# Kernel tuning notes

Hardware: AMD Instinct MI355X
Metric: run time of the kernel (lower is better)

Reference implementation:

```python
import jax, jax.numpy as jnp
import numpy as np

B, N, D, A = 256, 32, 128, 16
DOA, E, FD, H, O = 144, 128, 128, 256, 1  # obs_act_in, obs_out/embed, final_in, hidden, final_out


def setup_inputs() -> dict:
    key = jax.random.key(0)
    ks = jax.random.split(key, 12)
    p = lambda k, shape: jax.random.normal(k, shape, jnp.float32) * 0.05
    return {
        "states": jax.random.normal(ks[0], (B, N, D), jnp.float32),
        "policies": jax.random.uniform(ks[1], (B, N, A), dtype=jnp.float32),
        "actions": jax.random.uniform(ks[2], (B, N, A), dtype=jnp.float32),
        "Wk_proc": p(ks[3], (D, E)),
        "Wq_proc": p(ks[4], (D, E)),
        "Wv_proc": p(ks[5], (D, E)),
        "Wk": p(ks[6], (E, FD)),
        "Wq": p(ks[7], (E, FD)),
        "We": p(ks[8], (DOA, E)),
        "Wav": p(ks[9], (E, FD)),
        "W1": p(ks[10], (FD, H)),
        "W2": p(ks[11], (H, O)),
    }


def reference(states, policies, actions, Wk_proc, Wq_proc, Wv_proc, Wk, Wq, We, Wav, W1, W2):
    n = states.shape[1]
    # NOTE: original code divides BOTH attention stages by sqrt(self.d_k_obs) = final_input_dim
    scale = 1.0 / jnp.sqrt(jnp.asarray(Wk.shape[1], states.dtype))

    # stage-1 attention over agents [B,N,N]
    k1 = states @ Wk_proc
    q1 = states @ Wq_proc
    v1 = states @ Wv_proc
    w1 = jax.nn.softmax(jnp.einsum('bie,bje->bij', q1, k1) * scale, axis=-1)
    wav1 = jnp.einsum('bij,bje->bie', w1, v1)  # [B,N,E]

    # stage-2 attention weights
    k2 = wav1 @ Wk
    q2 = wav1 @ Wq
    w2 = jax.nn.softmax(jnp.einsum('bif,bjf->bij', q2, k2) * scale, axis=-1)

    # build obs-action/policy tensor: entry [b,i,j] uses policy of agent j when i==j else action of j
    oa = jnp.concatenate([states, actions], axis=-1)   # [B,N,DOA]
    op = jnp.concatenate([states, policies], axis=-1)  # [B,N,DOA]
    eye = jnp.eye(n, dtype=states.dtype)[:, :, None]   # [N,N,1]
    oap = eye * op[:, None, :, :] + (1.0 - eye) * oa[:, None, :, :]  # [B,N,N,DOA]

    av = (oap @ We) @ Wav  # [B,N,N,FD]

    # node_features[b,i,j,f] = sum_k w2[b,i,k] * av[b,j,k,f]  (avoids the 5D repeat)
    node = jnp.einsum('bik,bjkf->bijf', w2, av)

    h = node @ W1
    h = jnp.where(h > 0, h, 0.01 * h)  # leaky_relu, default slope
    value = h @ W2  # [B,N,N,O]
    return value, w1, w2
```

## Files before the change

### kernel.cpp

```cpp
#include <hip/hip_runtime.h>
#include <math.h>

#define NB 256
#define NN 32
#define DD 128
#define NA 16
#define HH 256

using f32x4v  = __attribute__((ext_vector_type(4))) float;
using bf16x8  = __attribute__((ext_vector_type(8))) short;

static __device__ __forceinline__ float4 ld4(const float* p){ return *reinterpret_cast<const float4*>(p); }
static __device__ __forceinline__ void st4f(float* p, float4 v){ *reinterpret_cast<float4*>(p) = v; }
static __device__ __forceinline__ float elem(float4 v, int kk){
    return (kk==0)?v.x:(kk==1)?v.y:(kk==2)?v.z:v.w;
}

static __device__ __forceinline__ unsigned f2bf(float x){
    unsigned u = __float_as_uint(x);
    u += 0x7fffu + ((u >> 16) & 1u);
    return u >> 16;
}
static __device__ __forceinline__ unsigned pack2(float a, float b){
    return f2bf(a) | (f2bf(b) << 16);
}

static __device__ __forceinline__ f32x4v mfma16(bf16x8 a, bf16x8 b, f32x4v c){
    return __builtin_amdgcn_mfma_f32_16x16x32_bf16(a, b, c, 0, 0, 0);
}

static __device__ __forceinline__ bf16x8 to_bf8(const float v[8]){
    union { bf16x8 v8; unsigned u[4]; } r;
    #pragma unroll
    for (int j = 0; j < 4; j++) r.u[j] = pack2(v[2*j], v[2*j+1]);
    return r.v8;
}

static __device__ __forceinline__ void store_frag(unsigned short* __restrict__ dst,
                                                  int frag, int l, const float v[8]){
    uint4 p;
    p.x = pack2(v[0], v[1]); p.y = pack2(v[2], v[3]);
    p.z = pack2(v[4], v[5]); p.w = pack2(v[6], v[7]);
    *reinterpret_cast<uint4*>(dst + (size_t)(frag*64 + l)*8) = p;
}

__global__ __launch_bounds__(512)
void k_pre(const float* __restrict__ We, const float* __restrict__ Wav,
           const float* __restrict__ W1,
           const float* __restrict__ Wqp, const float* __restrict__ Wkp,
           const float* __restrict__ Wvp, const float* __restrict__ Wq,
           const float* __restrict__ Wk,
           float* __restrict__ WABf, unsigned short* __restrict__ WABs,
           unsigned short* __restrict__ Wqps, unsigned short* __restrict__ Wkps,
           unsigned short* __restrict__ Wvqs, unsigned short* __restrict__ Wvks)
{
    __shared__ float SH[5120];
    const int t = threadIdx.x;
    const int bid = blockIdx.x;
    const int l   = t & 63;
    const int wvv = t >> 6;
    const int lg  = l >> 4;
    const int lc  = l & 15;

    if (bid < 16) {
        float* T2f  = SH;
        float* WABt = SH + 2560;
        const int ct = bid;
        {
            const int arow = wvv*16 + lc;
            f32x4v acc = {0.f,0.f,0.f,0.f};
            #pragma unroll
            for (int kt = 0; kt < 4; kt++) {
                const float* ap = Wav + (size_t)arow*128 + kt*32 + lg*8;
                float4 a0 = ld4(ap), a1 = ld4(ap + 4);
                float av8[8] = {a0.x,a0.y,a0.z,a0.w,a1.x,a1.y,a1.z,a1.w};
                const float* bp = W1 + (size_t)(kt*32 + lg*8)*256 + ct*16 + lc;
                float bv8[8];
                #pragma unroll
                for (int i = 0; i < 8; i++) bv8[i] = bp[(size_t)i*256];
                acc = mfma16(to_bf8(av8), to_bf8(bv8), acc);
            }
            const int dr = wvv*16 + lg*4;
            #pragma unroll
            for (int r = 0; r < 4; r++) T2f[(dr+r)*20 + lc] = acc[r];
        }
        __syncthreads();
        #pragma unroll
        for (int pass = 0; pass < 2; pass++) {
            const int mt9 = (pass == 0) ? wvv : 8 + wvv;
            if (pass == 1 && wvv >= 2) continue;
            const int arow = mt9*16 + lc;
            f32x4v acc = {0.f,0.f,0.f,0.f};
            #pragma unroll
            for (int kt = 0; kt < 4; kt++) {
                float av8[8];
                if (arow < 144) {
                    const float* ap = We + (size_t)arow*128 + kt*32 + lg*8;
                    float4 a0 = ld4(ap), a1 = ld4(ap + 4);
                    av8[0]=a0.x; av8[1]=a0.y; av8[2]=a0.z; av8[3]=a0.w;
                    av8[4]=a1.x; av8[5]=a1.y; av8[6]=a1.z; av8[7]=a1.w;
                } else {
                    #pragma unroll
                    for (int i = 0; i < 8; i++) av8[i] = 0.f;
                }
                float bv8[8];
                #pragma unroll
                for (int i = 0; i < 8; i++) bv8[i] = T2f[(kt*32 + lg*8 + i)*20 + lc];
                acc = mfma16(to_bf8(av8), to_bf8(bv8), acc);
            }
            const int dr = mt9*16 + lg*4;
            #pragma unroll
            for (int r = 0; r < 4; r++) WABt[(dr+r)*16 + lc] = acc[r];
            if (mt9 == 8) {
                #pragma unroll
                for (int r = 0; r < 4; r++)
                    WABf[(size_t)(dr+r)*256 + ct*16 + lc] = acc[r];
            }
        }
        __syncthreads();
        if (t < 320) {
            int kt = t >> 6, ll = t & 63;
            float v[8];
            #pragma unroll
            for (int i = 0; i < 8; i++)
                v[i] = WABt[(kt*32 + (ll>>4)*8 + i)*16 + (ll&15)];
            store_frag(WABs, kt*16 + ct, ll, v);
        }
    } else if (bid < 24) {
        const int bb = bid - 16;
        const int fg = bb*8 + (t >> 6);
        const int sel = fg >> 5, frag = fg & 31;
        const int kt = frag >> 3, nt = frag & 7;
        const float* W = (sel==0) ? Wqp : Wkp;
        unsigned short* dst = (sel==0) ? Wqps : Wkps;
        float v[8];
        #pragma unroll
        for (int i = 0; i < 8; i++)
            v[i] = W[(kt*32 + (l>>4)*8 + i)*128 + nt*16 + (l&15)];
        store_frag(dst, frag, l, v);
    } else {
        float* T2f = SH;
        const int ct = (bid - 24) & 7;
        const float* Bsrc = (bid < 32) ? Wq : Wk;
        unsigned short* dst = (bid < 32) ? Wvqs : Wvks;
        {
            const int arow = wvv*16 + lc;
            f32x4v acc = {0.f,0.f,0.f,0.f};
            #pragma unroll
            for (int kt = 0; kt < 4; kt++) {
                const float* ap = Wvp + (size_t)arow*128 + kt*32 + lg*8;
                float4 a0 = ld4(ap), a1 = ld4(ap + 4);
                float av8[8] = {a0.x,a0.y,a0.z,a0.w,a1.x,a1.y,a1.z,a1.w};
                const float* bp = Bsrc + (size_t)(kt*32 + lg*8)*128 + ct*16 + lc;
                float bv8[8];
                #pragma unroll
                for (int i = 0; i < 8; i++) bv8[i] = bp[(size_t)i*128];
                acc = mfma16(to_bf8(av8), to_bf8(bv8), acc);
            }
            const int dr = wvv*16 + lg*4;
            #pragma unroll
            for (int r = 0; r < 4; r++) T2f[(dr+r)*20 + lc] = acc[r];
        }
        __syncthreads();
        if (t < 256) {
            int kt = t >> 6, ll = t & 63;
            float v[8];
            #pragma unroll
            for (int i = 0; i < 8; i++)
                v[i] = T2f[(kt*32 + (ll>>4)*8 + i)*20 + (ll&15)];
            store_frag(dst, kt*8 + ct, ll, v);
        }
    }
}

static __device__ __forceinline__ void scores_softmax512(const float* __restrict__ Qm,
                                                         const float* __restrict__ Km,
                                                         float scale,
                                                         float* __restrict__ w_lds,
                                                         float* __restrict__ w_out,
                                                         int i, int j)
{
    float s0 = 0.f, s1 = 0.f;
    #pragma unroll 4
    for (int k=0;k<128;k+=4){
        float4 qv = ld4(Qm + i*132 + k);
        float4 k0 = ld4(Km + j*132 + k);
        float4 k1 = ld4(Km + (j+16)*132 + k);
        s0 += qv.x*k0.x + qv.y*k0.y + qv.z*k0.z + qv.w*k0.w;
        s1 += qv.x*k1.x + qv.y*k1.y + qv.z*k1.z + qv.w*k1.w;
    }
    s0 *= scale; s1 *= scale;
    float m = fmaxf(s0, s1);
    #pragma unroll
    for (int d=1; d<16; d<<=1) m = fmaxf(m, __shfl_xor(m, d));
    float e0 = expf(s0 - m), e1 = expf(s1 - m);
    float sum = e0 + e1;
    #pragma unroll
    for (int d=1; d<16; d<<=1) sum += __shfl_xor(sum, d);
    float inv = 1.f / sum;
    e0 *= inv; e1 *= inv;
    w_lds[i*36 + j]      = e0;
    w_lds[i*36 + j + 16] = e1;
    w_out[i*32 + j]      = e0;
    w_out[i*32 + j + 16] = e1;
}

__global__ __launch_bounds__(512)
void k_main(const float* __restrict__ states, const float* __restrict__ pol,
            const float* __restrict__ act,
            const unsigned short* __restrict__ Wqps, const unsigned short* __restrict__ Wkps,
            const unsigned short* __restrict__ Wvqs, const unsigned short* __restrict__ Wvks,
            const unsigned short* __restrict__ WABs, const float* __restrict__ WABf,
            const float* __restrict__ W2,
            float* __restrict__ out_v, float* __restrict__ out_w1,
            float* __restrict__ out_w2)
{
    const int b = blockIdx.x;
    const int t = threadIdx.x;
    const float scale = 0.08838834764831845f;

    __shared__ float SH[15360];
    float* B1   = SH;
    float* B2   = SH + 4224;
    float* Wb1f = SH + 8448;
    float* Wb2f = SH + 9600;
    float* APd  = SH + 10752;
    unsigned short* Xoa = (unsigned short*)(SH + 11264);
    float*    A1 = SH;
    unsigned* P2 = (unsigned*)(SH + 11264);
    unsigned* Q2 = (unsigned*)SH;
    float* SPQ = Wb1f;

    const float* stg  = states + (size_t)b*(NN*DD);
    const float* actg = act + (size_t)b*(NN*NA);
    const float* polg = pol + (size_t)b*(NN*NA);

    const int l   = t & 63;
    const int wvv = t >> 6;
    const int lg  = l >> 4;
    const int lc  = l & 15;

    {
        int r = t >> 4, kb = t & 15;
        #pragma unroll
        for (int uu = 0; uu < 10; uu++){
            int k = kb + 16*uu;
            float v = (k < 128) ? stg[r*128 + k]
                    : (k < 144) ? actg[r*16 + (k-128)] : 0.f;
            Xoa[r*168 + k] = (unsigned short)f2bf(v);
        }
        if (t < 128) {
            int rr = t>>2, cc = (t&3)*4;
            float4 p = ld4(polg + rr*16 + cc), a = ld4(actg + rr*16 + cc);
            st4f(APd + rr*16 + cc, make_float4(p.x-a.x, p.y-a.y, p.z-a.z, p.w-a.w));
        }
    }
    __syncthreads();

    const int mt   = wvv & 1;
    const int ntb  = (wvv >> 1) * 2;
    const int nb7  = (wvv >> 1) * 4;
    const int arow = mt*16 + lc;
    const int drow = mt*16 + (lg << 2);
    const int dcol = lc;
    const int c  = t & 127;
    const int g  = t >> 7;
    const int cp = (t & 127)*2;
    const int si = t >> 4;
    const int sj = t & 15;
    const int wp = wvv & 1;

    f32x4v asq0={0.f,0.f,0.f,0.f}, asq1={0.f,0.f,0.f,0.f};
    f32x4v ask0={0.f,0.f,0.f,0.f}, ask1={0.f,0.f,0.f,0.f};
    {
        f32x4v aq0={0.f,0.f,0.f,0.f}, aq1={0.f,0.f,0.f,0.f};
        f32x4v ak0={0.f,0.f,0.f,0.f}, ak1={0.f,0.f,0.f,0.f};
        const unsigned short* ab = Xoa + arow*168 + lg*8;
        #pragma unroll
        for (int kt = 0; kt < 4; kt++){
            bf16x8 a = *reinterpret_cast<const bf16x8*>(ab + kt*32);
            bf16x8 bq0 = *reinterpret_cast<const bf16x8*>(Wqps + (size_t)((kt*8+ntb  )*64 + l)*8);
            bf16x8 bq1 = *reinterpret_cast<const bf16x8*>(Wqps + (size_t)((kt*8+ntb+1)*64 + l)*8);
            bf16x8 bk0 = *reinterpret_cast<const bf16x8*>(Wkps + (size_t)((kt*8+ntb  )*64 + l)*8);
            bf16x8 bk1 = *reinterpret_cast<const bf16x8*>(Wkps + (size_t)((kt*8+ntb+1)*64 + l)*8);
            bf16x8 bv0 = *reinterpret_cast<const bf16x8*>(Wvqs + (size_t)((kt*8+ntb  )*64 + l)*8);
            bf16x8 bv1 = *reinterpret_cast<const bf16x8*>(Wvqs + (size_t)((kt*8+ntb+1)*64 + l)*8);
            bf16x8 bw0 = *reinterpret_cast<const bf16x8*>(Wvks + (size_t)((kt*8+ntb  )*64 + l)*8);
            bf16x8 bw1 = *reinterpret_cast<const bf16x8*>(Wvks + (size_t)((kt*8+ntb+1)*64 + l)*8);
            aq0 = mfma16(a, bq0, aq0); aq1 = mfma16(a, bq1, aq1);
            ak0 = mfma16(a, bk0, ak0); ak1 = mfma16(a, bk1, ak1);
            asq0 = mfma16(a, bv0, asq0); asq1 = mfma16(a, bv1, asq1);
            ask0 = mfma16(a, bw0, ask0); ask1 = mfma16(a, bw1, ask1);
        }
        #pragma unroll
        for (int r = 0; r < 4; r++){
            B1[(drow+r)*132 + ntb*16     + dcol] = aq0[r];
            B1[(drow+r)*132 + (ntb+1)*16 + dcol] = aq1[r];
            B2[(drow+r)*132 + ntb*16     + dcol] = ak0[r];
            B2[(drow+r)*132 + (ntb+1)*16 + dcol] = ak1[r];
        }
    }
    __syncthreads();

    scores_softmax512(B1, B2, scale, Wb1f, out_w1 + (size_t)b*1024, si, sj);
    __syncthreads();

    #pragma unroll
    for (int r = 0; r < 4; r++){
        B1[(drow+r)*132 + ntb*16     + dcol] = asq0[r];
        B1[(drow+r)*132 + (ntb+1)*16 + dcol] = asq1[r];
        B2[(drow+r)*132 + ntb*16     + dcol] = ask0[r];
        B2[(drow+r)*132 + (ntb+1)*16 + dcol] = ask1[r];
    }
    __syncthreads();

    {
        float q2a[8], k2a[8];
        #pragma unroll
        for (int u=0;u<8;u++){ q2a[u]=0.f; k2a[u]=0.f; }
        #pragma unroll
        for (int k0=0;k0<32;k0+=4){
            float4 xv[8];
            #pragma unroll
            for (int u=0;u<8;u++) xv[u] = ld4(Wb1f + (g*8+u)*36 + k0);
            #pragma unroll
            for (int kk=0;kk<4;kk++){
                float vq = B1[(k0+kk)*132 + c];
                float vk = B2[(k0+kk)*132 + c];
                #pragma unroll
                for (int u=0;u<8;u++){
                    float x = elem(xv[u],kk);
                    q2a[u] = fmaf(x, vq, q2a[u]);
                    k2a[u] = fmaf(x, vk, k2a[u]);
                }
            }
        }
        __syncthreads();
        #pragma unroll
        for (int u=0;u<8;u++){
            B1[(g*8+u)*132 + c] = q2a[u];
            B2[(g*8+u)*132 + c] = k2a[u];
        }
    }
    __syncthreads();

    scores_softmax512(B1, B2, scale, Wb2f, out_w2 + (size_t)b*1024, si, sj);
    __syncthreads();

    {
        f32x4v ac[4];
        #pragma unroll
        for (int n=0;n<4;n++) ac[n] = f32x4v{0.f,0.f,0.f,0.f};
        const unsigned short* ab = Xoa + arow*168 + lg*8;
        #pragma unroll
        for (int kt = 0; kt < 5; kt++){
            bf16x8 a = *reinterpret_cast<const bf16x8*>(ab + kt*32);
            #pragma unroll
            for (int n = 0; n < 4; n++){
                bf16x8 bb = *reinterpret_cast<const bf16x8*>(WABs + (size_t)((kt*16 + nb7 + n)*64 + l)*8);
                ac[n] = mfma16(a, bb, ac[n]);
            }
        }
        #pragma unroll
        for (int n = 0; n < 4; n++){
            #pragma unroll
            for (int r = 0; r < 4; r++)
                A1[(drow+r)*260 + (nb7+n)*16 + dcol] = ac[n][r];
        }
    }
    __syncthreads();

    {
        float ap0[8], ap1[8];
        #pragma unroll
        for (int u=0;u<8;u++){ ap0[u]=0.f; ap1[u]=0.f; }
        #pragma unroll
        for (int k0=0;k0<32;k0+=4){
            float4 xv[8];
            #pragma unroll
            for (int u=0;u<8;u++) xv[u] = ld4(Wb2f + (g*8+u)*36 + k0);
            #pragma unroll
            for (int kk=0;kk<4;kk++){
                float2 w = *reinterpret_cast<const float2*>(A1 + (k0+kk)*260 + cp);
                #pragma unroll
                for (int u=0;u<8;u++){
                    float x = elem(xv[u],kk);
                    ap0[u] = fmaf(x, w.x, ap0[u]);
                    ap1[u] = fmaf(x, w.y, ap1[u]);
                }
            }
        }
        #pragma unroll
        for (int u=0;u<8;u++)
            P2[(g*8+u)*128 + (cp>>1)] = pack2(ap0[u], ap1[u]);
        float2 w2v = *reinterpret_cast<const float2*>(W2 + cp);
        float sp[8];
        #pragma unroll
        for (int u=0;u<8;u++) sp[u] = ap0[u]*w2v.x + ap1[u]*w2v.y;
        #pragma unroll
        for (int d=1; d<64; d<<=1){
            #pragma unroll
            for (int u=0;u<8;u++) sp[u] += __shfl_xor(sp[u], d);
        }
        if (l == 0){
            #pragma unroll
            for (int u=0;u<8;u++) SPQ[(g*8+u)*2 + wp] = sp[u];
        }
    }
    __syncthreads();

    {
        float aq0[8], aq1[8];
        #pragma unroll
        for (int u=0;u<8;u++){ aq0[u]=0.f; aq1[u]=0.f; }
        const float* wB = WABf + 128*256;
        #pragma unroll
        for (int k0=0;k0<16;k0+=4){
            float4 xv[8];
            #pragma unroll
            for (int u=0;u<8;u++) xv[u] = ld4(APd + (g*8+u)*16 + k0);
            #pragma unroll
            for (int kk=0;kk<4;kk++){
                float2 w = *reinterpret_cast<const float2*>(wB + (k0+kk)*256 + cp);
                #pragma unroll
                for (int u=0;u<8;u++){
                    float x = elem(xv[u],kk);
                    aq0[u] = fmaf(x, w.x, aq0[u]);
                    aq1[u] = fmaf(x, w.y, aq1[u]);
                }
            }
        }
        #pragma unroll
        for (int u=0;u<8;u++)
            Q2[(g*8+u)*132 + (cp>>1)] = pack2(aq0[u], aq1[u]);
        float2 w2v = *reinterpret_cast<const float2*>(W2 + cp);
        float sq[8];
        #pragma unroll
        for (int u=0;u<8;u++) sq[u] = aq0[u]*w2v.x + aq1[u]*w2v.y;
        #pragma unroll
        for (int d=1; d<64; d<<=1){
            #pragma unroll
            for (int u=0;u<8;u++) sq[u] += __shfl_xor(sq[u], d);
        }
        if (l == 0){
            #pragma unroll
            for (int u=0;u<8;u++) SPQ[64 + (g*8+u)*2 + wp] = sq[u];
        }
    }
    __syncthreads();

    {
        float w00 = Wb2f[si*36 + sj], w01 = Wb2f[si*36 + sj + 16];
        float SPi = SPQ[si*2] + SPQ[si*2+1];
        float SQa = SPQ[64 + sj*2] + SPQ[64 + sj*2+1];
        float SQb = SPQ[64 + (sj+16)*2] + SPQ[64 + (sj+16)*2+1];
        float a0 = 0.f, a1 = 0.f;

        #define PROC(PA,QA,QB,H2) {                                         \
            float w2e = W2[(H2)], w2o = W2[(H2)+1];                         \
            float paE = __uint_as_float((PA)<<16), paO = __uint_as_float((PA) & 0xffff0000u); \
            float qaE = __uint_as_float((QA)<<16), qaO = __uint_as_float((QA) & 0xffff0000u); \
            float qbE = __uint_as_float((QB)<<16), qbO = __uint_as_float((QB) & 0xffff0000u); \
            float t0 = fmaf(w00, qaE, paE); a0 = fmaf(fabsf(t0), w2e, a0);  \
            float t1 = fmaf(w00, qaO, paO); a0 = fmaf(fabsf(t1), w2o, a0);  \
            float t2 = fmaf(w01, qbE, paE); a1 = fmaf(fabsf(t2), w2e, a1);  \
            float t3 = fmaf(w01, qbO, paO); a1 = fmaf(fabsf(t3), w2o, a1); }

        #pragma unroll 4
        for (int hp4 = 0; hp4 < 32; hp4++){
            uint4 pa4 = *reinterpret_cast<const uint4*>(P2 + si*128 + hp4*4);
            uint4 qa4 = *reinterpret_cast<const uint4*>(Q2 + sj*132 + hp4*4);
            uint4 qb4 = *reinterpret_cast<const uint4*>(Q2 + (sj+16)*132 + hp4*4);
            PROC(pa4.x, qa4.x, qb4.x, hp4*8+0)
            PROC(pa4.y, qa4.y, qb4.y, hp4*8+2)
            PROC(pa4.z, qa4.z, qb4.z, hp4*8+4)
            PROC(pa4.w, qa4.w, qb4.w, hp4*8+6)
        }
        #undef PROC

        float* ov = out_v + (size_t)b*1024;
        ov[si*32 + sj]      = fmaf(0.495f, a0, 0.505f*(SPi + w00*SQa));
        ov[si*32 + sj + 16] = fmaf(0.495f, a1, 0.505f*(SPi + w01*SQb));
    }
}

extern "C" void kernel_launch(void* const* d_in, const int* in_sizes, int n_in,
                              void* d_out, int out_size, void* d_ws, size_t ws_size,
                              hipStream_t stream) {
    const float* states = (const float*)d_in[0];
    const float* pol    = (const float*)d_in[1];
    const float* act    = (const float*)d_in[2];
    const float* Wkp    = (const float*)d_in[3];
    const float* Wqp    = (const float*)d_in[4];
    const float* Wvp    = (const float*)d_in[5];
    const float* Wk     = (const float*)d_in[6];
    const float* Wq     = (const float*)d_in[7];
    const float* We     = (const float*)d_in[8];
    const float* Wav    = (const float*)d_in[9];
    const float* W1     = (const float*)d_in[10];
    const float* W2     = (const float*)d_in[11];

    float* out    = (float*)d_out;
    float* out_v  = out;
    float* out_w1 = out + 256*1024;
    float* out_w2 = out + 2*256*1024;

    float* WABf = (float*)d_ws;
    unsigned short* WABs = (unsigned short*)(WABf + 36864);
    unsigned short* wsu  = (unsigned short*)(WABf + 57344);
    unsigned short* Wqps = wsu;
    unsigned short* Wkps = wsu + 16384;
    unsigned short* Wvqs = wsu + 32768;
    unsigned short* Wvks = wsu + 49152;

    hipLaunchKernelGGL(k_pre, dim3(40), dim3(512), 0, stream,
                       We, Wav, W1, Wqp, Wkp, Wvp, Wq, Wk,
                       WABf, WABs, Wqps, Wkps, Wvqs, Wvks);
    hipLaunchKernelGGL(k_main, dim3(NB), dim3(512), 0, stream,
                       states, pol, act,
                       Wqps, Wkps, Wvqs, Wvks, WABs, WABf, W2,
                       out_v, out_w1, out_w2);
}
```

Before: 38.41 us.

## Double k_main block size to 1024 threads, halving per-thread work

```diff
diff --git a/kernel.cpp b/kernel.cpp
--- a/kernel.cpp
+++ b/kernel.cpp
@@ -173,39 +173,34 @@
     }
 }
 
-static __device__ __forceinline__ void scores_softmax512(const float* __restrict__ Qm,
-                                                         const float* __restrict__ Km,
-                                                         float scale,
-                                                         float* __restrict__ w_lds,
-                                                         float* __restrict__ w_out,
-                                                         int i, int j)
+static __device__ __forceinline__ void scores_softmax1024(const float* __restrict__ Qm,
+                                                          const float* __restrict__ Km,
+                                                          float scale,
+                                                          float* __restrict__ w_lds,
+                                                          float* __restrict__ w_out,
+                                                          int i, int j)
 {
-    float s0 = 0.f, s1 = 0.f;
+    float s0 = 0.f;
     #pragma unroll 4
     for (int k=0;k<128;k+=4){
         float4 qv = ld4(Qm + i*132 + k);
         float4 k0 = ld4(Km + j*132 + k);
-        float4 k1 = ld4(Km + (j+16)*132 + k);
         s0 += qv.x*k0.x + qv.y*k0.y + qv.z*k0.z + qv.w*k0.w;
-        s1 += qv.x*k1.x + qv.y*k1.y + qv.z*k1.z + qv.w*k1.w;
-    }
-    s0 *= scale; s1 *= scale;
-    float m = fmaxf(s0, s1);
+    }
+    s0 *= scale;
+    float m = s0;
     #pragma unroll
-    for (int d=1; d<16; d<<=1) m = fmaxf(m, __shfl_xor(m, d));
-    float e0 = expf(s0 - m), e1 = expf(s1 - m);
-    float sum = e0 + e1;
+    for (int d=1; d<32; d<<=1) m = fmaxf(m, __shfl_xor(m, d));
+    float e0 = expf(s0 - m);
+    float sum = e0;
     #pragma unroll
-    for (int d=1; d<16; d<<=1) sum += __shfl_xor(sum, d);
-    float inv = 1.f / sum;
-    e0 *= inv; e1 *= inv;
-    w_lds[i*36 + j]      = e0;
-    w_lds[i*36 + j + 16] = e1;
-    w_out[i*32 + j]      = e0;
-    w_out[i*32 + j + 16] = e1;
-}
-
-__global__ __launch_bounds__(512)
+    for (int d=1; d<32; d<<=1) sum += __shfl_xor(sum, d);
+    float w = e0 / sum;
+    w_lds[i*36 + j] = w;
+    w_out[i*32 + j] = w;
+}
+
+__global__ __launch_bounds__(1024)
 void k_main(const float* __restrict__ states, const float* __restrict__ pol,
             const float* __restrict__ act,
             const unsigned short* __restrict__ Wqps, const unsigned short* __restrict__ Wkps,
@@ -241,10 +236,10 @@
     const int lc  = l & 15;
 
     {
-        int r = t >> 4, kb = t & 15;
-        #pragma unroll
-        for (int uu = 0; uu < 10; uu++){
-            int k = kb + 16*uu;
+        int r = t >> 5, kb = t & 31;
+        #pragma unroll
+        for (int uu = 0; uu < 5; uu++){
+            int k = kb + 32*uu;
             float v = (k < 128) ? stg[r*128 + k]
                     : (k < 144) ? actg[r*16 + (k-128)] : 0.f;
             Xoa[r*168 + k] = (unsigned short)f2bf(v);
@@ -258,77 +253,69 @@
     __syncthreads();
 
     const int mt   = wvv & 1;
-    const int ntb  = (wvv >> 1) * 2;
-    const int nb7  = (wvv >> 1) * 4;
+    const int ntb  = wvv >> 1;
+    const int nb7  = (wvv >> 1) * 2;
     const int arow = mt*16 + lc;
     const int drow = mt*16 + (lg << 2);
     const int dcol = lc;
     const int c  = t & 127;
     const int g  = t >> 7;
     const int cp = (t & 127)*2;
-    const int si = t >> 4;
-    const int sj = t & 15;
+    const int si = t >> 5;
+    const int sj = t & 31;
     const int wp = wvv & 1;
 
-    f32x4v asq0={0.f,0.f,0.f,0.f}, asq1={0.f,0.f,0.f,0.f};
-    f32x4v ask0={0.f,0.f,0.f,0.f}, ask1={0.f,0.f,0.f,0.f};
-    {
-        f32x4v aq0={0.f,0.f,0.f,0.f}, aq1={0.f,0.f,0.f,0.f};
-        f32x4v ak0={0.f,0.f,0.f,0.f}, ak1={0.f,0.f,0.f,0.f};
+    f32x4v asq0={0.f,0.f,0.f,0.f};
+    f32x4v ask0={0.f,0.f,0.f,0.f};
+    {
+        f32x4v aq0={0.f,0.f,0.f,0.f};
+        f32x4v ak0={0.f,0.f,0.f,0.f};
         const unsigned short* ab = Xoa + arow*168 + lg*8;
         #pragma unroll
         for (int kt = 0; kt < 4; kt++){
             bf16x8 a = *reinterpret_cast<const bf16x8*>(ab + kt*32);
-            bf16x8 bq0 = *reinterpret_cast<const bf16x8*>(Wqps + (size_t)((kt*8+ntb  )*64 + l)*8);
-            bf16x8 bq1 = *reinterpret_cast<const bf16x8*>(Wqps + (size_t)((kt*8+ntb+1)*64 + l)*8);
-            bf16x8 bk0 = *reinterpret_cast<const bf16x8*>(Wkps + (size_t)((kt*8+ntb  )*64 + l)*8);
-            bf16x8 bk1 = *reinterpret_cast<const bf16x8*>(Wkps + (size_t)((kt*8+ntb+1)*64 + l)*8);
-            bf16x8 bv0 = *reinterpret_cast<const bf16x8*>(Wvqs + (size_t)((kt*8+ntb  )*64 + l)*8);
-            bf16x8 bv1 = *reinterpret_cast<const bf16x8*>(Wvqs + (size_t)((kt*8+ntb+1)*64 + l)*8);
-            bf16x8 bw0 = *reinterpret_cast<const bf16x8*>(Wvks + (size_t)((kt*8+ntb  )*64 + l)*8);
-            bf16x8 bw1 = *reinterpret_cast<const bf16x8*>(Wvks + (size_t)((kt*8+ntb+1)*64 + l)*8);
-            aq0 = mfma16(a, bq0, aq0); aq1 = mfma16(a, bq1, aq1);
-            ak0 = mfma16(a, bk0, ak0); ak1 = mfma16(a, bk1, ak1);
-            asq0 = mfma16(a, bv0, asq0); asq1 = mfma16(a, bv1, asq1);
-            ask0 = mfma16(a, bw0, ask0); ask1 = mfma16(a, bw1, ask1);
+            bf16x8 bq0 = *reinterpret_cast<const bf16x8*>(Wqps + (size_t)((kt*8+ntb)*64 + l)*8);
+            bf16x8 bk0 = *reinterpret_cast<const bf16x8*>(Wkps + (size_t)((kt*8+ntb)*64 + l)*8);
+            bf16x8 bv0 = *reinterpret_cast<const bf16x8*>(Wvqs + (size_t)((kt*8+ntb)*64 + l)*8);
+            bf16x8 bw0 = *reinterpret_cast<const bf16x8*>(Wvks + (size_t)((kt*8+ntb)*64 + l)*8);
+            aq0 = mfma16(a, bq0, aq0);
+            ak0 = mfma16(a, bk0, ak0);
+            asq0 = mfma16(a, bv0, asq0);
+            ask0 = mfma16(a, bw0, ask0);
         }
         #pragma unroll
         for (int r = 0; r < 4; r++){
-            B1[(drow+r)*132 + ntb*16     + dcol] = aq0[r];
-            B1[(drow+r)*132 + (ntb+1)*16 + dcol] = aq1[r];
-            B2[(drow+r)*132 + ntb*16     + dcol] = ak0[r];
-            B2[(drow+r)*132 + (ntb+1)*16 + dcol] = ak1[r];
-        }
-    }
-    __syncthreads();
-
-    scores_softmax512(B1, B2, scale, Wb1f, out_w1 + (size_t)b*1024, si, sj);
+            B1[(drow+r)*132 + ntb*16 + dcol] = aq0[r];
+            B2[(drow+r)*132 + ntb*16 + dcol] = ak0[r];
+        }
+    }
+    __syncthreads();
+
+    scores_softmax1024(B1, B2, scale, Wb1f, out_w1 + (size_t)b*1024, si, sj);
     __syncthreads();
 
     #pragma unroll
     for (int r = 0; r < 4; r++){
-        B1[(drow+r)*132 + ntb*16     + dcol] = asq0[r];
-        B1[(drow+r)*132 + (ntb+1)*16 + dcol] = asq1[r];
-        B2[(drow+r)*132 + ntb*16     + dcol] = ask0[r];
-        B2[(drow+r)*132 + (ntb+1)*16 + dcol] = ask1[r];
-    }
-    __syncthreads();
-
-    {
-        float q2a[8], k2a[8];
-        #pragma unroll
-        for (int u=0;u<8;u++){ q2a[u]=0.f; k2a[u]=0.f; }
+        B1[(drow+r)*132 + ntb*16 + dcol] = asq0[r];
+        B2[(drow+r)*132 + ntb*16 + dcol] = ask0[r];
+    }
+    __syncthreads();
+
+    {
+        float q2a[4], k2a[4];
+        #pragma unroll
+        for (int u=0;u<4;u++){ q2a[u]=0.f; k2a[u]=0.f; }
         #pragma unroll
         for (int k0=0;k0<32;k0+=4){
-            float4 xv[8];
-            #pragma unroll
-            for (int u=0;u<8;u++) xv[u] = ld4(Wb1f + (g*8+u)*36 + k0);
+            float4 xv[4];
+            #pragma unroll
+            for (int u=0;u<4;u++) xv[u] = ld4(Wb1f + (g*4+u)*36 + k0);
             #pragma unroll
             for (int kk=0;kk<4;kk++){
                 float vq = B1[(k0+kk)*132 + c];
                 float vk = B2[(k0+kk)*132 + c];
                 #pragma unroll
-                for (int u=0;u<8;u++){
+                for (int u=0;u<4;u++){
                     float x = elem(xv[u],kk);
                     q2a[u] = fmaf(x, vq, q2a[u]);
                     k2a[u] = fmaf(x, vk, k2a[u]);
@@ -337,32 +324,32 @@
         }
         __syncthreads();
         #pragma unroll
-        for (int u=0;u<8;u++){
-            B1[(g*8+u)*132 + c] = q2a[u];
-            B2[(g*8+u)*132 + c] = k2a[u];
-        }
-    }
-    __syncthreads();
-
-    scores_softmax512(B1, B2, scale, Wb2f, out_w2 + (size_t)b*1024, si, sj);
-    __syncthreads();
-
-    {
-        f32x4v ac[4];
-        #pragma unroll
-        for (int n=0;n<4;n++) ac[n] = f32x4v{0.f,0.f,0.f,0.f};
+        for (int u=0;u<4;u++){
+            B1[(g*4+u)*132 + c] = q2a[u];
+            B2[(g*4+u)*132 + c] = k2a[u];
+        }
+    }
+    __syncthreads();
+
+    scores_softmax1024(B1, B2, scale, Wb2f, out_w2 + (size_t)b*1024, si, sj);
+    __syncthreads();
+
+    {
+        f32x4v ac[2];
+        #pragma unroll
+        for (int n=0;n<2;n++) ac[n] = f32x4v{0.f,0.f,0.f,0.f};
         const unsigned short* ab = Xoa + arow*168 + lg*8;
         #pragma unroll
         for (int kt = 0; kt < 5; kt++){
             bf16x8 a = *reinterpret_cast<const bf16x8*>(ab + kt*32);
             #pragma unroll
-            for (int n = 0; n < 4; n++){
+            for (int n = 0; n < 2; n++){
                 bf16x8 bb = *reinterpret_cast<const bf16x8*>(WABs + (size_t)((kt*16 + nb7 + n)*64 + l)*8);
                 ac[n] = mfma16(a, bb, ac[n]);
             }
         }
         #pragma unroll
-        for (int n = 0; n < 4; n++){
+        for (int n = 0; n < 2; n++){
             #pragma unroll
             for (int r = 0; r < 4; r++)
                 A1[(drow+r)*260 + (nb7+n)*16 + dcol] = ac[n][r];
@@ -371,19 +358,19 @@
     __syncthreads();
 
     {
-        float ap0[8], ap1[8];
-        #pragma unroll
-        for (int u=0;u<8;u++){ ap0[u]=0.f; ap1[u]=0.f; }
+        float ap0[4], ap1[4];
+        #pragma unroll
+        for (int u=0;u<4;u++){ ap0[u]=0.f; ap1[u]=0.f; }
         #pragma unroll
         for (int k0=0;k0<32;k0+=4){
-            float4 xv[8];
-            #pragma unroll
-            for (int u=0;u<8;u++) xv[u] = ld4(Wb2f + (g*8+u)*36 + k0);
+            float4 xv[4];
+            #pragma unroll
+            for (int u=0;u<4;u++) xv[u] = ld4(Wb2f + (g*4+u)*36 + k0);
             #pragma unroll
             for (int kk=0;kk<4;kk++){
                 float2 w = *reinterpret_cast<const float2*>(A1 + (k0+kk)*260 + cp);
                 #pragma unroll
-                for (int u=0;u<8;u++){
+                for (int u=0;u<4;u++){
                     float x = elem(xv[u],kk);
                     ap0[u] = fmaf(x, w.x, ap0[u]);
                     ap1[u] = fmaf(x, w.y, ap1[u]);
@@ -391,39 +378,39 @@
             }
         }
         #pragma unroll
-        for (int u=0;u<8;u++)
-            P2[(g*8+u)*128 + (cp>>1)] = pack2(ap0[u], ap1[u]);
+        for (int u=0;u<4;u++)
+            P2[(g*4+u)*128 + (cp>>1)] = pack2(ap0[u], ap1[u]);
         float2 w2v = *reinterpret_cast<const float2*>(W2 + cp);
-        float sp[8];
-        #pragma unroll
-        for (int u=0;u<8;u++) sp[u] = ap0[u]*w2v.x + ap1[u]*w2v.y;
+        float sp[4];
+        #pragma unroll
+        for (int u=0;u<4;u++) sp[u] = ap0[u]*w2v.x + ap1[u]*w2v.y;
         #pragma unroll
         for (int d=1; d<64; d<<=1){
             #pragma unroll
-            for (int u=0;u<8;u++) sp[u] += __shfl_xor(sp[u], d);
+            for (int u=0;u<4;u++) sp[u] += __shfl_xor(sp[u], d);
         }
         if (l == 0){
             #pragma unroll
-            for (int u=0;u<8;u++) SPQ[(g*8+u)*2 + wp] = sp[u];
-        }
-    }
-    __syncthreads();
-
-    {
-        float aq0[8], aq1[8];
-        #pragma unroll
-        for (int u=0;u<8;u++){ aq0[u]=0.f; aq1[u]=0.f; }
+            for (int u=0;u<4;u++) SPQ[(g*4+u)*2 + wp] = sp[u];
+        }
+    }
+    __syncthreads();
+
+    {
+        float aq0[4], aq1[4];
+        #pragma unroll
+        for (int u=0;u<4;u++){ aq0[u]=0.f; aq1[u]=0.f; }
         const float* wB = WABf + 128*256;
         #pragma unroll
         for (int k0=0;k0<16;k0+=4){
-            float4 xv[8];
-            #pragma unroll
-            for (int u=0;u<8;u++) xv[u] = ld4(APd + (g*8+u)*16 + k0);
+            float4 xv[4];
+            #pragma unroll
+            for (int u=0;u<4;u++) xv[u] = ld4(APd + (g*4+u)*16 + k0);
             #pragma unroll
             for (int kk=0;kk<4;kk++){
                 float2 w = *reinterpret_cast<const float2*>(wB + (k0+kk)*256 + cp);
                 #pragma unroll
-                for (int u=0;u<8;u++){
+                for (int u=0;u<4;u++){
                     float x = elem(xv[u],kk);
                     aq0[u] = fmaf(x, w.x, aq0[u]);
                     aq1[u] = fmaf(x, w.y, aq1[u]);
@@ -431,56 +418,49 @@
             }
         }
         #pragma unroll
-        for (int u=0;u<8;u++)
-            Q2[(g*8+u)*132 + (cp>>1)] = pack2(aq0[u], aq1[u]);
+        for (int u=0;u<4;u++)
+            Q2[(g*4+u)*132 + (cp>>1)] = pack2(aq0[u], aq1[u]);
         float2 w2v = *reinterpret_cast<const float2*>(W2 + cp);
-        float sq[8];
-        #pragma unroll
-        for (int u=0;u<8;u++) sq[u] = aq0[u]*w2v.x + aq1[u]*w2v.y;
+        float sq[4];
+        #pragma unroll
+        for (int u=0;u<4;u++) sq[u] = aq0[u]*w2v.x + aq1[u]*w2v.y;
         #pragma unroll
         for (int d=1; d<64; d<<=1){
             #pragma unroll
-            for (int u=0;u<8;u++) sq[u] += __shfl_xor(sq[u], d);
+            for (int u=0;u<4;u++) sq[u] += __shfl_xor(sq[u], d);
         }
         if (l == 0){
             #pragma unroll
-            for (int u=0;u<8;u++) SPQ[64 + (g*8+u)*2 + wp] = sq[u];
-        }
-    }
-    __syncthreads();
-
-    {
-        float w00 = Wb2f[si*36 + sj], w01 = Wb2f[si*36 + sj + 16];
+            for (int u=0;u<4;u++) SPQ[64 + (g*4+u)*2 + wp] = sq[u];
+        }
+    }
+    __syncthreads();
+
+    {
+        float w00 = Wb2f[si*36 + sj];
         float SPi = SPQ[si*2] + SPQ[si*2+1];
         float SQa = SPQ[64 + sj*2] + SPQ[64 + sj*2+1];
-        float SQb = SPQ[64 + (sj+16)*2] + SPQ[64 + (sj+16)*2+1];
-        float a0 = 0.f, a1 = 0.f;
-
-        #define PROC(PA,QA,QB,H2) {                                         \
+        float a0 = 0.f;
+
+        #define PROC(PA,QA,H2) {                                            \
             float w2e = W2[(H2)], w2o = W2[(H2)+1];                         \
             float paE = __uint_as_float((PA)<<16), paO = __uint_as_float((PA) & 0xffff0000u); \
             float qaE = __uint_as_float((QA)<<16), qaO = __uint_as_float((QA) & 0xffff0000u); \
-            float qbE = __uint_as_float((QB)<<16), qbO = __uint_as_float((QB) & 0xffff0000u); \
             float t0 = fmaf(w00, qaE, paE); a0 = fmaf(fabsf(t0), w2e, a0);  \
-            float t1 = fmaf(w00, qaO, paO); a0 = fmaf(fabsf(t1), w2o, a0);  \
-            float t2 = fmaf(w01, qbE, paE); a1 = fmaf(fabsf(t2), w2e, a1);  \
-            float t3 = fmaf(w01, qbO, paO); a1 = fmaf(fabsf(t3), w2o, a1); }
+            float t1 = fmaf(w00, qaO, paO); a0 = fmaf(fabsf(t1), w2o, a0); }
 
         #pragma unroll 4
         for (int hp4 = 0; hp4 < 32; hp4++){
             uint4 pa4 = *reinterpret_cast<const uint4*>(P2 + si*128 + hp4*4);
             uint4 qa4 = *reinterpret_cast<const uint4*>(Q2 + sj*132 + hp4*4);
-            uint4 qb4 = *reinterpret_cast<const uint4*>(Q2 + (sj+16)*132 + hp4*4);
-            PROC(pa4.x, qa4.x, qb4.x, hp4*8+0)
-            PROC(pa4.y, qa4.y, qb4.y, hp4*8+2)
-            PROC(pa4.z, qa4.z, qb4.z, hp4*8+4)
-            PROC(pa4.w, qa4.w, qb4.w, hp4*8+6)
+            PROC(pa4.x, qa4.x, hp4*8+0)
+            PROC(pa4.y, qa4.y, hp4*8+2)
+            PROC(pa4.z, qa4.z, hp4*8+4)
+            PROC(pa4.w, qa4.w, hp4*8+6)
         }
         #undef PROC
 
-        float* ov = out_v + (size_t)b*1024;
-        ov[si*32 + sj]      = fmaf(0.495f, a0, 0.505f*(SPi + w00*SQa));
-        ov[si*32 + sj + 16] = fmaf(0.495f, a1, 0.505f*(SPi + w01*SQb));
+        out_v[(size_t)b*1024 + si*32 + sj] = fmaf(0.495f, a0, 0.505f*(SPi + w00*SQa));
     }
 }
 
@@ -516,7 +496,7 @@
     hipLaunchKernelGGL(k_pre, dim3(40), dim3(512), 0, stream,
                        We, Wav, W1, Wqp, Wkp, Wvp, Wq, Wk,
                        WABf, WABs, Wqps, Wkps, Wvqs, Wvks);
-    hipLaunchKernelGGL(k_main, dim3(NB), dim3(512), 0, stream,
+    hipLaunchKernelGGL(k_main, dim3(NB), dim3(1024), 0, stream,
                        states, pol, act,
                        Wqps, Wkps, Wvqs, Wvks, WABs, WABf, W2,
                        out_v, out_w1, out_w2);
```

Measured after the change: 36.49 us. 5.0% less time.
